# Performance work log

Hardware: AMD Instinct MI355X
Metric: run time of the kernel (lower is better)

The kernel has to match this reference:

```python
import jax, jax.numpy as jnp
import numpy as np

EMB_DIM = 1024
HEAD_DIM = 64
NUM_HEADS = EMB_DIM // HEAD_DIM  # 16
BATCH = 2
SEQ = 2048


def setup_inputs() -> dict:
    key = jax.random.key(0)
    ks = jax.random.split(key, 8)
    s = 0.02
    return {
        "q": jax.random.normal(ks[0], (BATCH, SEQ, EMB_DIM), dtype=jnp.float32),
        "k": jax.random.normal(ks[1], (BATCH, SEQ, EMB_DIM), dtype=jnp.float32),
        "v": jax.random.normal(ks[2], (BATCH, SEQ, EMB_DIM), dtype=jnp.float32),
        "W_q": jax.random.normal(ks[3], (HEAD_DIM, HEAD_DIM), dtype=jnp.float32) * s,
        "W_k": jax.random.normal(ks[4], (HEAD_DIM, HEAD_DIM), dtype=jnp.float32) * s,
        "W_v": jax.random.normal(ks[5], (HEAD_DIM, HEAD_DIM), dtype=jnp.float32) * s,
        "W_fc": jax.random.normal(ks[6], (EMB_DIM, EMB_DIM), dtype=jnp.float32) * s,
        "b_fc": jax.random.normal(ks[7], (EMB_DIM,), dtype=jnp.float32) * s,
    }


def reference(q, k, v, W_q, W_k, W_v, W_fc, b_fc):
    b = v.shape[0]
    # split into heads: [B, S, H, D]
    qh = q.reshape(b, -1, NUM_HEADS, HEAD_DIM)
    kh = k.reshape(b, -1, NUM_HEADS, HEAD_DIM)
    vh = v.reshape(b, -1, NUM_HEADS, HEAD_DIM)
    # per-head shared projections (nn.Linear: x @ W.T, no bias)
    qh = jnp.einsum('bshd,ed->bshe', qh, W_q)
    kh = jnp.einsum('bshd,ed->bshe', kh, W_k)
    vh = jnp.einsum('bshd,ed->bshe', vh, W_v)
    # scores: [B, Q, K, H]
    attn = jnp.einsum('nqhd,nkhd->nqkh', qh, kh)
    # NOTE (faithful to source): softmax over the HEADS axis (dim=3),
    # and scale by sqrt(emb_dim), not sqrt(head_dim).
    attn = jax.nn.softmax(attn / jnp.sqrt(jnp.float32(EMB_DIM)), axis=3)
    # weighted values: [B, Q, H, D] -> [B, Q, EMB]
    out = jnp.einsum('nqkh,nkhd->nqhd', attn, vh).reshape(b, -1, EMB_DIM)
    return out @ W_fc.T + b_fc
```

## Files before the change

### kernel.cpp

```cpp
#include <hip/hip_runtime.h>
#include <hip/hip_bf16.h>

#define S_LEN 2048
#define NHEAD 16
#define HDIM 64
#define EMB 1024

typedef short v8s __attribute__((ext_vector_type(8)));
typedef float v4f __attribute__((ext_vector_type(4)));

__device__ __forceinline__ float bflo(unsigned u) {
    union { unsigned u; float f; } v; v.u = u << 16; return v.f;
}
__device__ __forceinline__ float bfhi(unsigned u) {
    union { unsigned u; float f; } v; v.u = u & 0xFFFF0000u; return v.f;
}
__device__ __forceinline__ unsigned cvtpk(float lo, float hi) {
    union { __hip_bfloat162 h2; unsigned u; } v;
    float2 f; f.x = lo; f.y = hi;
    v.h2 = __float22bfloat162_rn(f);
    return v.u;
}
__device__ __forceinline__ unsigned short f2bf(float f) {
    return (unsigned short)cvtpk(f, f);
}
__device__ __forceinline__ v8s cvt8(float4 a, float4 b) {
    v8s r;
    ((unsigned*)&r)[0] = cvtpk(a.x, a.y);
    ((unsigned*)&r)[1] = cvtpk(a.z, a.w);
    ((unsigned*)&r)[2] = cvtpk(b.x, b.y);
    ((unsigned*)&r)[3] = cvtpk(b.z, b.w);
    return r;
}

__global__ __launch_bounds__(128) void k_proj2(
    const float* __restrict__ q, const float* __restrict__ k, const float* __restrict__ v,
    const float* __restrict__ Wq, const float* __restrict__ Wk, const float* __restrict__ Wv,
    unsigned short* __restrict__ Qp, unsigned short* __restrict__ Kp, unsigned short* __restrict__ Vt)
{
    __shared__ unsigned short Tq[2][16][72];
    const int t = threadIdx.x, wave = t >> 6, lane = t & 63;
    const int l15 = lane & 15, l4 = lane >> 4;
    const int mtx = blockIdx.y;
    const int hq = blockIdx.z;
    const int row0 = blockIdx.x * 32 + wave * 16;
    const int b = row0 >> 11, s0 = row0 & 2047;
    const float* X = (mtx == 0) ? q : (mtx == 1) ? k : v;
    const float* W = (mtx == 0) ? Wq : (mtx == 1) ? Wk : Wv;

    v8s wf[4][2];
    #pragma unroll
    for (int tile = 0; tile < 4; ++tile)
        #pragma unroll
        for (int c2 = 0; c2 < 2; ++c2) {
            const float* wp = W + (tile * 16 + l15) * 64 + c2 * 32 + l4 * 8;
            wf[tile][c2] = cvt8(*(const float4*)wp, *(const float4*)(wp + 4));
        }

    #pragma unroll
    for (int hi = 0; hi < 4; ++hi) {
        const int h = hq * 4 + hi;
        v8s xf[2];
        #pragma unroll
        for (int c2 = 0; c2 < 2; ++c2) {
            const float* xp = X + (size_t)(row0 + l15) * EMB + h * 64 + c2 * 32 + l4 * 8;
            xf[c2] = cvt8(*(const float4*)xp, *(const float4*)(xp + 4));
        }
        v4f acc[4];
        #pragma unroll
        for (int i = 0; i < 4; ++i) acc[i] = (v4f){0.f, 0.f, 0.f, 0.f};
        if (mtx < 2) {
            #pragma unroll
            for (int ns = 0; ns < 4; ++ns)
                #pragma unroll
                for (int c2 = 0; c2 < 2; ++c2)
                    acc[ns] = __builtin_amdgcn_mfma_f32_16x16x32_bf16(xf[c2], wf[ns][c2], acc[ns], 0, 0, 0);
            #pragma unroll
            for (int ns = 0; ns < 4; ++ns)
                #pragma unroll
                for (int r = 0; r < 4; ++r)
                    Tq[wave][l4 * 4 + r][ns * 16 + l15] = f2bf(acc[ns][r]);
            const int row = lane >> 2, c8 = (lane & 3) * 16;
            uint4 d0 = *(const uint4*)&Tq[wave][row][c8];
            uint4 d1 = *(const uint4*)&Tq[wave][row][c8 + 8];
            unsigned short* dst = ((mtx == 0) ? Qp : Kp)
                + (size_t)(b * NHEAD + h) * S_LEN * HDIM + (size_t)(s0 + row) * HDIM + c8;
            *(uint4*)dst = d0;
            *(uint4*)(dst + 8) = d1;
        } else {
            #pragma unroll
            for (int ms = 0; ms < 4; ++ms)
                #pragma unroll
                for (int c2 = 0; c2 < 2; ++c2)
                    acc[ms] = __builtin_amdgcn_mfma_f32_16x16x32_bf16(wf[ms][c2], xf[c2], acc[ms], 0, 0, 0);
            unsigned short* dst = Vt + (size_t)(b * NHEAD + h) * HDIM * S_LEN;
            #pragma unroll
            for (int ms = 0; ms < 4; ++ms)
                #pragma unroll
                for (int r = 0; r < 4; ++r)
                    dst[(size_t)(ms * 16 + l4 * 4 + r) * S_LEN + s0 + l15] = f2bf(acc[ms][r]);
        }
    }
}

__global__ __launch_bounds__(256) void k_cvtw(
    const float* __restrict__ W, unsigned short* __restrict__ Wb)
{
    const int i = (blockIdx.x * 256 + threadIdx.x) * 4;
    float4 wv = *(const float4*)(W + i);
    uint2 pk;
    pk.x = cvtpk(wv.x, wv.y);
    pk.y = cvtpk(wv.z, wv.w);
    *(uint2*)(Wb + i) = pk;
}

__global__ __launch_bounds__(1024, 4) void k_fattn(
    const unsigned short* __restrict__ Qp, const unsigned short* __restrict__ Kp,
    const unsigned short* __restrict__ Vt, unsigned short* __restrict__ Op)
{
    __shared__ unsigned short Pex[16][64][40];
    __shared__ unsigned ZrsU[64][20];
    const int t = threadIdx.x, wave = t >> 6, lane = t & 63;
    const int l15 = lane & 15, l4 = lane >> 4;
    const int h = wave;
    const int id = blockIdx.x;
    const int slot = id & 7;
    const int kqb = slot & 3;
    const int bsel = slot >> 2;
    const int qt = bsel * 32 + (id >> 3);
    const int b = qt >> 5;
    const int q0 = (qt & 31) * 64;
    const unsigned short* qh = Qp + (size_t)(b * NHEAD + h) * S_LEN * HDIM;
    const unsigned short* kh = Kp + (size_t)(b * NHEAD + h) * S_LEN * HDIM;
    const unsigned short* vh = Vt + (size_t)(b * NHEAD + h) * HDIM * S_LEN;

    v8s aq[4][2];
    #pragma unroll
    for (int qs = 0; qs < 4; ++qs)
        #pragma unroll
        for (int c2 = 0; c2 < 2; ++c2)
            aq[qs][c2] = *(const v8s*)(qh + (size_t)(q0 + qs * 16 + l15) * HDIM + c2 * 32 + l4 * 8);

    v4f o[4][4];
    #pragma unroll
    for (int qs = 0; qs < 4; ++qs)
        #pragma unroll
        for (int ds = 0; ds < 4; ++ds)
            o[qs][ds] = (v4f){0.f, 0.f, 0.f, 0.f};

    const int zq = t >> 4;
    const int zc = t & 15;

    for (int c = 0; c < 16; ++c) {
        const int kk0 = kqb * 512 + c * 32;
        #pragma unroll
        for (int ks = 0; ks < 2; ++ks) {
            const unsigned short* kb = kh + (size_t)(kk0 + ks * 16 + l15) * HDIM + l4 * 8;
            v8s b0 = *(const v8s*)kb;
            v8s b1 = *(const v8s*)(kb + 32);
            #pragma unroll
            for (int qs = 0; qs < 4; ++qs) {
                v4f sf = (v4f){0.f, 0.f, 0.f, 0.f};
                sf = __builtin_amdgcn_mfma_f32_16x16x32_bf16(aq[qs][0], b0, sf, 0, 0, 0);
                sf = __builtin_amdgcn_mfma_f32_16x16x32_bf16(aq[qs][1], b1, sf, 0, 0, 0);
                const int rb = qs * 16 + l4 * 4;
                unsigned p01 = cvtpk(__expf(sf[0] * 0.03125f), __expf(sf[1] * 0.03125f));
                unsigned p23 = cvtpk(__expf(sf[2] * 0.03125f), __expf(sf[3] * 0.03125f));
                Pex[h][rb + 0][ks * 16 + l15] = (unsigned short)p01;
                Pex[h][rb + 1][ks * 16 + l15] = (unsigned short)(p01 >> 16);
                Pex[h][rb + 2][ks * 16 + l15] = (unsigned short)p23;
                Pex[h][rb + 3][ks * 16 + l15] = (unsigned short)(p23 >> 16);
            }
        }
        __syncthreads();
        {
            float z0 = 0.f, z1 = 0.f;
            #pragma unroll
            for (int hh = 0; hh < 16; ++hh) {
                unsigned u = *(const unsigned*)&Pex[hh][zq][zc * 2];
                z0 += bflo(u); z1 += bfhi(u);
            }
            ZrsU[zq][zc] = cvtpk(__builtin_amdgcn_rcpf(z0), __builtin_amdgcn_rcpf(z1));
        }
        __syncthreads();
        {
            v8s bv[4];
            #pragma unroll
            for (int ds = 0; ds < 4; ++ds)
                bv[ds] = *(const v8s*)(vh + (size_t)(ds * 16 + l15) * S_LEN + kk0 + l4 * 8);
            #pragma unroll
            for (int qs = 0; qs < 4; ++qs) {
                uint4 pu = *(const uint4*)&Pex[h][qs * 16 + l15][l4 * 8];
                uint4 zv = *(const uint4*)&ZrsU[qs * 16 + l15][l4 * 4];
                v8s pn;
                ((unsigned*)&pn)[0] = cvtpk(bflo(pu.x) * bflo(zv.x), bfhi(pu.x) * bfhi(zv.x));
                ((unsigned*)&pn)[1] = cvtpk(bflo(pu.y) * bflo(zv.y), bfhi(pu.y) * bfhi(zv.y));
                ((unsigned*)&pn)[2] = cvtpk(bflo(pu.z) * bflo(zv.z), bfhi(pu.z) * bfhi(zv.z));
                ((unsigned*)&pn)[3] = cvtpk(bflo(pu.w) * bflo(zv.w), bfhi(pu.w) * bfhi(zv.w));
                #pragma unroll
                for (int ds = 0; ds < 4; ++ds)
                    o[qs][ds] = __builtin_amdgcn_mfma_f32_16x16x32_bf16(pn, bv[ds], o[qs][ds], 0, 0, 0);
            }
        }
    }

    unsigned short* op = Op + (size_t)(kqb * 2 + b) * S_LEN * EMB;
    #pragma unroll
    for (int qs = 0; qs < 4; ++qs)
        #pragma unroll
        for (int ds = 0; ds < 4; ++ds)
            #pragma unroll
            for (int r = 0; r < 4; ++r)
                op[(size_t)(q0 + qs * 16 + l4 * 4 + r) * EMB + h * 64 + ds * 16 + l15] =
                    f2bf(o[qs][ds][r]);
}

__global__ __launch_bounds__(256) void k_merge4(
    const unsigned short* __restrict__ Op, unsigned short* __restrict__ AO)
{
    const size_t i = ((size_t)blockIdx.x * 256 + threadIdx.x) * 8;
    const size_t row = i >> 10;
    const int b = (int)(row >> 11);
    const size_t off = (row & 2047) * EMB + (i & 1023);
    float a0 = 0, a1 = 0, a2 = 0, a3 = 0, a4 = 0, a5 = 0, a6 = 0, a7 = 0;
    #pragma unroll
    for (int kq = 0; kq < 4; ++kq) {
        uint4 u = *(const uint4*)(Op + (size_t)(kq * 2 + b) * S_LEN * EMB + off);
        a0 += bflo(u.x); a1 += bfhi(u.x);
        a2 += bflo(u.y); a3 += bfhi(u.y);
        a4 += bflo(u.z); a5 += bfhi(u.z);
        a6 += bflo(u.w); a7 += bfhi(u.w);
    }
    uint4 r;
    r.x = cvtpk(a0, a1); r.y = cvtpk(a2, a3);
    r.z = cvtpk(a4, a5); r.w = cvtpk(a6, a7);
    *(uint4*)(AO + i) = r;
}

__global__ __launch_bounds__(256) void k_fc(
    const unsigned short* __restrict__ AO, const unsigned short* __restrict__ Wb,
    const float* __restrict__ bias, float* __restrict__ out)
{
    const int t = threadIdx.x, wave = t >> 6, lane = t & 63;
    const int l15 = lane & 15, l4 = lane >> 4;
    const int m0 = blockIdx.x * 128 + wave * 32;
    const int n0 = blockIdx.y * 64;
    v4f c[2][4];
    #pragma unroll
    for (int i = 0; i < 2; ++i)
        #pragma unroll
        for (int j = 0; j < 4; ++j) c[i][j] = (v4f){0.f, 0.f, 0.f, 0.f};
    for (int k = 0; k < EMB; k += 32) {
        v8s a0 = *(const v8s*)(AO + (size_t)(m0 + l15) * EMB + k + l4 * 8);
        v8s a1 = *(const v8s*)(AO + (size_t)(m0 + 16 + l15) * EMB + k + l4 * 8);
        #pragma unroll
        for (int ns = 0; ns < 4; ++ns) {
            v8s bw = *(const v8s*)(Wb + (size_t)(n0 + ns * 16 + l15) * EMB + k + l4 * 8);
            c[0][ns] = __builtin_amdgcn_mfma_f32_16x16x32_bf16(a0, bw, c[0][ns], 0, 0, 0);
            c[1][ns] = __builtin_amdgcn_mfma_f32_16x16x32_bf16(a1, bw, c[1][ns], 0, 0, 0);
        }
    }
    #pragma unroll
    for (int ms = 0; ms < 2; ++ms)
        #pragma unroll
        for (int ns = 0; ns < 4; ++ns) {
            const float bv = bias[n0 + ns * 16 + l15];
            #pragma unroll
            for (int r = 0; r < 4; ++r)
                out[(size_t)(m0 + ms * 16 + l4 * 4 + r) * EMB + n0 + ns * 16 + l15] = c[ms][ns][r] + bv;
        }
}

extern "C" void kernel_launch(void* const* d_in, const int* in_sizes, int n_in,
                              void* d_out, int out_size, void* d_ws, size_t ws_size,
                              hipStream_t stream)
{
    (void)in_sizes; (void)n_in; (void)out_size; (void)ws_size;
    const float* q   = (const float*)d_in[0];
    const float* k   = (const float*)d_in[1];
    const float* v   = (const float*)d_in[2];
    const float* Wq  = (const float*)d_in[3];
    const float* Wk  = (const float*)d_in[4];
    const float* Wv  = (const float*)d_in[5];
    const float* Wfc = (const float*)d_in[6];
    const float* bfc = (const float*)d_in[7];

    char* w = (char*)d_ws;
    unsigned short* Qp = (unsigned short*)(w);
    unsigned short* Kp = (unsigned short*)(w + (8u  << 20));
    unsigned short* Vt = (unsigned short*)(w + (16u << 20));
    unsigned short* Wb = (unsigned short*)(w + (24u << 20));
    unsigned short* Op = (unsigned short*)(w + (26u << 20));
    unsigned short* AO = Qp;

    k_proj2 <<<dim3(128, 3, 4), dim3(128),  0, stream>>>(q, k, v, Wq, Wk, Wv, Qp, Kp, Vt);
    k_cvtw  <<<dim3(1024),      dim3(256),  0, stream>>>(Wfc, Wb);
    k_fattn <<<dim3(256),       dim3(1024), 0, stream>>>(Qp, Kp, Vt, Op);
    k_merge4<<<dim3(2048),      dim3(256),  0, stream>>>(Op, AO);
    k_fc    <<<dim3(32, 16),    dim3(256),  0, stream>>>(AO, Wb, bfc, (float*)d_out);
}
```

Baseline: 278.2 us.

## Software-pipeline attention across double-buffered query halves to overlap cross-head softmax

Each 32-key chunk is split into two 32-row query halves, each with its own LDS buffer for the exponentials and the head-sum reciprocals. The schedule becomes a software pipeline: the P·V MFMAs for one half, the cross-head normalisation for the other half and the QK exponentials for the next half run between single barriers. This removes the separate barrier that used to isolate the reduction step and lets MFMA work overlap with LDS reduction. In exchange, V tiles are now loaded from global memory once per half, so twice per chunk, and only 512 threads do the reduction.

After: 347.5 us. 24.9% more time.

```diff
diff --git a/kernel.cpp b/kernel.cpp
--- a/kernel.cpp
+++ b/kernel.cpp
@@ -118,8 +118,8 @@
     const unsigned short* __restrict__ Qp, const unsigned short* __restrict__ Kp,
     const unsigned short* __restrict__ Vt, unsigned short* __restrict__ Op)
 {
-    __shared__ unsigned short Pex[16][64][40];
-    __shared__ unsigned ZrsU[64][20];
+    __shared__ unsigned short Pex[2][16][32][40];
+    __shared__ unsigned ZrsU[2][32][20];
     const int t = threadIdx.x, wave = t >> 6, lane = t & 63;
     const int l15 = lane & 15, l4 = lane >> 4;
     const int h = wave;
@@ -148,10 +148,7 @@
         for (int ds = 0; ds < 4; ++ds)
             o[qs][ds] = (v4f){0.f, 0.f, 0.f, 0.f};
 
-    const int zq = t >> 4;
-    const int zc = t & 15;
-
-    for (int c = 0; c < 16; ++c) {
+    auto PH1 = [&](int qa, int c) {
         const int kk0 = kqb * 512 + c * 32;
         #pragma unroll
         for (int ks = 0; ks < 2; ++ks) {
@@ -159,50 +156,72 @@
             v8s b0 = *(const v8s*)kb;
             v8s b1 = *(const v8s*)(kb + 32);
             #pragma unroll
-            for (int qs = 0; qs < 4; ++qs) {
+            for (int qh2 = 0; qh2 < 2; ++qh2) {
                 v4f sf = (v4f){0.f, 0.f, 0.f, 0.f};
-                sf = __builtin_amdgcn_mfma_f32_16x16x32_bf16(aq[qs][0], b0, sf, 0, 0, 0);
-                sf = __builtin_amdgcn_mfma_f32_16x16x32_bf16(aq[qs][1], b1, sf, 0, 0, 0);
-                const int rb = qs * 16 + l4 * 4;
+                sf = __builtin_amdgcn_mfma_f32_16x16x32_bf16(aq[qa * 2 + qh2][0], b0, sf, 0, 0, 0);
+                sf = __builtin_amdgcn_mfma_f32_16x16x32_bf16(aq[qa * 2 + qh2][1], b1, sf, 0, 0, 0);
+                const int rb = qh2 * 16 + l4 * 4;
                 unsigned p01 = cvtpk(__expf(sf[0] * 0.03125f), __expf(sf[1] * 0.03125f));
                 unsigned p23 = cvtpk(__expf(sf[2] * 0.03125f), __expf(sf[3] * 0.03125f));
-                Pex[h][rb + 0][ks * 16 + l15] = (unsigned short)p01;
-                Pex[h][rb + 1][ks * 16 + l15] = (unsigned short)(p01 >> 16);
-                Pex[h][rb + 2][ks * 16 + l15] = (unsigned short)p23;
-                Pex[h][rb + 3][ks * 16 + l15] = (unsigned short)(p23 >> 16);
+                Pex[qa][h][rb + 0][ks * 16 + l15] = (unsigned short)p01;
+                Pex[qa][h][rb + 1][ks * 16 + l15] = (unsigned short)(p01 >> 16);
+                Pex[qa][h][rb + 2][ks * 16 + l15] = (unsigned short)p23;
+                Pex[qa][h][rb + 3][ks * 16 + l15] = (unsigned short)(p23 >> 16);
             }
         }
+    };
+    auto PH2 = [&](int ba) {
+        if (t < 512) {
+            const int zq = t >> 4, zc = t & 15;
+            float z0a = 0.f, z0b = 0.f, z1a = 0.f, z1b = 0.f;
+            #pragma unroll
+            for (int hh = 0; hh < 16; hh += 2) {
+                unsigned ua = *(const unsigned*)&Pex[ba][hh][zq][zc * 2];
+                unsigned ub = *(const unsigned*)&Pex[ba][hh + 1][zq][zc * 2];
+                z0a += bflo(ua); z1a += bfhi(ua);
+                z0b += bflo(ub); z1b += bfhi(ub);
+            }
+            ZrsU[ba][zq][zc] = cvtpk(__builtin_amdgcn_rcpf(z0a + z0b),
+                                     __builtin_amdgcn_rcpf(z1a + z1b));
+        }
+    };
+    auto PH3 = [&](int qa, int c) {
+        const int kk0 = kqb * 512 + c * 32;
+        v8s pn[2];
+        #pragma unroll
+        for (int qh2 = 0; qh2 < 2; ++qh2) {
+            uint4 pu = *(const uint4*)&Pex[qa][h][qh2 * 16 + l15][l4 * 8];
+            uint4 zv = *(const uint4*)&ZrsU[qa][qh2 * 16 + l15][l4 * 4];
+            ((unsigned*)&pn[qh2])[0] = cvtpk(bflo(pu.x) * bflo(zv.x), bfhi(pu.x) * bfhi(zv.x));
+            ((unsigned*)&pn[qh2])[1] = cvtpk(bflo(pu.y) * bflo(zv.y), bfhi(pu.y) * bfhi(zv.y));
+            ((unsigned*)&pn[qh2])[2] = cvtpk(bflo(pu.z) * bflo(zv.z), bfhi(pu.z) * bfhi(zv.z));
+            ((unsigned*)&pn[qh2])[3] = cvtpk(bflo(pu.w) * bflo(zv.w), bfhi(pu.w) * bfhi(zv.w));
+        }
+        #pragma unroll
+        for (int ds = 0; ds < 4; ++ds) {
+            v8s bv = *(const v8s*)(vh + (size_t)(ds * 16 + l15) * S_LEN + kk0 + l4 * 8);
+            o[qa * 2 + 0][ds] = __builtin_amdgcn_mfma_f32_16x16x32_bf16(pn[0], bv, o[qa * 2 + 0][ds], 0, 0, 0);
+            o[qa * 2 + 1][ds] = __builtin_amdgcn_mfma_f32_16x16x32_bf16(pn[1], bv, o[qa * 2 + 1][ds], 0, 0, 0);
+        }
+    };
+
+    PH1(0, 0);
+    __syncthreads();
+    PH2(0);
+    PH1(1, 0);
+    __syncthreads();
+    #pragma unroll 2
+    for (int s = 1; s < 31; ++s) {
+        const int ba = s & 1, qo = 1 - ba;
+        PH3(qo, (s - 1) >> 1);
+        PH2(ba);
+        PH1(qo, (s + 1) >> 1);
         __syncthreads();
-        {
-            float z0 = 0.f, z1 = 0.f;
-            #pragma unroll
-            for (int hh = 0; hh < 16; ++hh) {
-                unsigned u = *(const unsigned*)&Pex[hh][zq][zc * 2];
-                z0 += bflo(u); z1 += bfhi(u);
-            }
-            ZrsU[zq][zc] = cvtpk(__builtin_amdgcn_rcpf(z0), __builtin_amdgcn_rcpf(z1));
-        }
-        __syncthreads();
-        {
-            v8s bv[4];
-            #pragma unroll
-            for (int ds = 0; ds < 4; ++ds)
-                bv[ds] = *(const v8s*)(vh + (size_t)(ds * 16 + l15) * S_LEN + kk0 + l4 * 8);
-            #pragma unroll
-            for (int qs = 0; qs < 4; ++qs) {
-                uint4 pu = *(const uint4*)&Pex[h][qs * 16 + l15][l4 * 8];
-                uint4 zv = *(const uint4*)&ZrsU[qs * 16 + l15][l4 * 4];
-                v8s pn;
-                ((unsigned*)&pn)[0] = cvtpk(bflo(pu.x) * bflo(zv.x), bfhi(pu.x) * bfhi(zv.x));
-                ((unsigned*)&pn)[1] = cvtpk(bflo(pu.y) * bflo(zv.y), bfhi(pu.y) * bfhi(zv.y));
-                ((unsigned*)&pn)[2] = cvtpk(bflo(pu.z) * bflo(zv.z), bfhi(pu.z) * bfhi(zv.z));
-                ((unsigned*)&pn)[3] = cvtpk(bflo(pu.w) * bflo(zv.w), bfhi(pu.w) * bfhi(zv.w));
-                #pragma unroll
-                for (int ds = 0; ds < 4; ++ds)
-                    o[qs][ds] = __builtin_amdgcn_mfma_f32_16x16x32_bf16(pn, bv[ds], o[qs][ds], 0, 0, 0);
-            }
-        }
     }
+    PH3(0, 15);
+    PH2(1);
+    __syncthreads();
+    PH3(1, 15);
 
     unsigned short* op = Op + (size_t)(kqb * 2 + b) * S_LEN * EMB;
     #pragma unroll
```

## Fuse split-K merge into FC GEMM and weight conversion into projection

Applied to the files above, without the earlier changes.

The separate merge kernel that summed four partial attention outputs is removed. The FC GEMM now loads the four bf16 partials directly and sums them while building its A fragments. The FC weight conversion moves into extra blocks of the projection kernel, which drops two launches and the AO round-trip through memory. In exchange, each FC block re-reads and re-sums the partials once per N tile (16 times), so A-operand traffic and ALU work inside the GEMM go up.

After: 317.6 us. 1.14x slower.

```diff
diff --git a/kernel.cpp b/kernel.cpp
--- a/kernel.cpp
+++ b/kernel.cpp
@@ -36,12 +36,29 @@
 __global__ __launch_bounds__(128) void k_proj2(
     const float* __restrict__ q, const float* __restrict__ k, const float* __restrict__ v,
     const float* __restrict__ Wq, const float* __restrict__ Wk, const float* __restrict__ Wv,
-    unsigned short* __restrict__ Qp, unsigned short* __restrict__ Kp, unsigned short* __restrict__ Vt)
+    const float* __restrict__ Wfc,
+    unsigned short* __restrict__ Qp, unsigned short* __restrict__ Kp,
+    unsigned short* __restrict__ Vt, unsigned short* __restrict__ Wb)
 {
     __shared__ unsigned short Tq[2][16][72];
     const int t = threadIdx.x, wave = t >> 6, lane = t & 63;
+    const int mtx = blockIdx.y;
+
+    if (mtx == 3) {
+        const int bi = blockIdx.x * 4 + blockIdx.z;
+        const int i = (bi * 128 + t) * 16;
+        #pragma unroll
+        for (int j = 0; j < 16; j += 4) {
+            float4 wv = *(const float4*)(Wfc + i + j);
+            uint2 pk;
+            pk.x = cvtpk(wv.x, wv.y);
+            pk.y = cvtpk(wv.z, wv.w);
+            *(uint2*)(Wb + i + j) = pk;
+        }
+        return;
+    }
+
     const int l15 = lane & 15, l4 = lane >> 4;
-    const int mtx = blockIdx.y;
     const int hq = blockIdx.z;
     const int row0 = blockIdx.x * 32 + wave * 16;
     const int b = row0 >> 11, s0 = row0 & 2047;
@@ -101,17 +118,6 @@
                     dst[(size_t)(ms * 16 + l4 * 4 + r) * S_LEN + s0 + l15] = f2bf(acc[ms][r]);
         }
     }
-}
-
-__global__ __launch_bounds__(256) void k_cvtw(
-    const float* __restrict__ W, unsigned short* __restrict__ Wb)
-{
-    const int i = (blockIdx.x * 256 + threadIdx.x) * 4;
-    float4 wv = *(const float4*)(W + i);
-    uint2 pk;
-    pk.x = cvtpk(wv.x, wv.y);
-    pk.y = cvtpk(wv.z, wv.w);
-    *(uint2*)(Wb + i) = pk;
 }
 
 __global__ __launch_bounds__(1024, 4) void k_fattn(
@@ -215,44 +221,43 @@
                     f2bf(o[qs][ds][r]);
 }
 
-__global__ __launch_bounds__(256) void k_merge4(
-    const unsigned short* __restrict__ Op, unsigned short* __restrict__ AO)
-{
-    const size_t i = ((size_t)blockIdx.x * 256 + threadIdx.x) * 8;
-    const size_t row = i >> 10;
-    const int b = (int)(row >> 11);
-    const size_t off = (row & 2047) * EMB + (i & 1023);
-    float a0 = 0, a1 = 0, a2 = 0, a3 = 0, a4 = 0, a5 = 0, a6 = 0, a7 = 0;
-    #pragma unroll
-    for (int kq = 0; kq < 4; ++kq) {
-        uint4 u = *(const uint4*)(Op + (size_t)(kq * 2 + b) * S_LEN * EMB + off);
-        a0 += bflo(u.x); a1 += bfhi(u.x);
-        a2 += bflo(u.y); a3 += bfhi(u.y);
-        a4 += bflo(u.z); a5 += bfhi(u.z);
-        a6 += bflo(u.w); a7 += bfhi(u.w);
-    }
-    uint4 r;
-    r.x = cvtpk(a0, a1); r.y = cvtpk(a2, a3);
-    r.z = cvtpk(a4, a5); r.w = cvtpk(a6, a7);
-    *(uint4*)(AO + i) = r;
+__device__ __forceinline__ v8s ld_sum4(const unsigned short* __restrict__ p) {
+    const size_t po = (size_t)2 * S_LEN * EMB;
+    uint4 u0 = *(const uint4*)(p);
+    uint4 u1 = *(const uint4*)(p + po);
+    uint4 u2 = *(const uint4*)(p + 2 * po);
+    uint4 u3 = *(const uint4*)(p + 3 * po);
+    v8s r;
+    ((unsigned*)&r)[0] = cvtpk(bflo(u0.x) + bflo(u1.x) + bflo(u2.x) + bflo(u3.x),
+                               bfhi(u0.x) + bfhi(u1.x) + bfhi(u2.x) + bfhi(u3.x));
+    ((unsigned*)&r)[1] = cvtpk(bflo(u0.y) + bflo(u1.y) + bflo(u2.y) + bflo(u3.y),
+                               bfhi(u0.y) + bfhi(u1.y) + bfhi(u2.y) + bfhi(u3.y));
+    ((unsigned*)&r)[2] = cvtpk(bflo(u0.z) + bflo(u1.z) + bflo(u2.z) + bflo(u3.z),
+                               bfhi(u0.z) + bfhi(u1.z) + bfhi(u2.z) + bfhi(u3.z));
+    ((unsigned*)&r)[3] = cvtpk(bflo(u0.w) + bflo(u1.w) + bflo(u2.w) + bflo(u3.w),
+                               bfhi(u0.w) + bfhi(u1.w) + bfhi(u2.w) + bfhi(u3.w));
+    return r;
 }
 
 __global__ __launch_bounds__(256) void k_fc(
-    const unsigned short* __restrict__ AO, const unsigned short* __restrict__ Wb,
+    const unsigned short* __restrict__ Op, const unsigned short* __restrict__ Wb,
     const float* __restrict__ bias, float* __restrict__ out)
 {
     const int t = threadIdx.x, wave = t >> 6, lane = t & 63;
     const int l15 = lane & 15, l4 = lane >> 4;
     const int m0 = blockIdx.x * 128 + wave * 32;
     const int n0 = blockIdx.y * 64;
+    const int b = m0 >> 11;
+    const int s0 = m0 & 2047;
+    const unsigned short* pa = Op + (size_t)b * S_LEN * EMB;
     v4f c[2][4];
     #pragma unroll
     for (int i = 0; i < 2; ++i)
         #pragma unroll
         for (int j = 0; j < 4; ++j) c[i][j] = (v4f){0.f, 0.f, 0.f, 0.f};
     for (int k = 0; k < EMB; k += 32) {
-        v8s a0 = *(const v8s*)(AO + (size_t)(m0 + l15) * EMB + k + l4 * 8);
-        v8s a1 = *(const v8s*)(AO + (size_t)(m0 + 16 + l15) * EMB + k + l4 * 8);
+        v8s a0 = ld_sum4(pa + (size_t)(s0 + l15) * EMB + k + l4 * 8);
+        v8s a1 = ld_sum4(pa + (size_t)(s0 + 16 + l15) * EMB + k + l4 * 8);
         #pragma unroll
         for (int ns = 0; ns < 4; ++ns) {
             v8s bw = *(const v8s*)(Wb + (size_t)(n0 + ns * 16 + l15) * EMB + k + l4 * 8);
@@ -291,11 +296,8 @@
     unsigned short* Vt = (unsigned short*)(w + (16u << 20));
     unsigned short* Wb = (unsigned short*)(w + (24u << 20));
     unsigned short* Op = (unsigned short*)(w + (26u << 20));
-    unsigned short* AO = Qp;
-
-    k_proj2 <<<dim3(128, 3, 4), dim3(128),  0, stream>>>(q, k, v, Wq, Wk, Wv, Qp, Kp, Vt);
-    k_cvtw  <<<dim3(1024),      dim3(256),  0, stream>>>(Wfc, Wb);
+
+    k_proj2 <<<dim3(128, 4, 4), dim3(128),  0, stream>>>(q, k, v, Wq, Wk, Wv, Wfc, Qp, Kp, Vt, Wb);
     k_fattn <<<dim3(256),       dim3(1024), 0, stream>>>(Qp, Kp, Vt, Op);
-    k_merge4<<<dim3(2048),      dim3(256),  0, stream>>>(Op, AO);
-    k_fc    <<<dim3(32, 16),    dim3(256),  0, stream>>>(AO, Wb, bfc, (float*)d_out);
-}
+    k_fc    <<<dim3(32, 16),    dim3(256),  0, stream>>>(Op, Wb, bfc, (float*)d_out);
+}
```

## Fold FC weight conversion into projection kernel and shrink FC tiles

Applied to the files above, without the earlier changes.

Removes the separate weight-cast kernel launch by giving the projection kernel an extra grid slice (mtx==3) that converts W_fc to bf16. Each of the 512 extra blocks converts 2048 elements, which covers the full 1024x1024 matrix. The shared staging buffer is given a per-head slot so the four head iterations no longer reuse the same LDS region. The FC GEMM tile is halved to 16 rows per wave, doubling the grid to raise occupancy and parallelism, at the cost of reloading the weight tile in twice as many blocks.

New measurement: 304.0 us. 9.3% more time.

```diff
diff --git a/kernel.cpp b/kernel.cpp
--- a/kernel.cpp
+++ b/kernel.cpp
@@ -36,12 +36,29 @@
 __global__ __launch_bounds__(128) void k_proj2(
     const float* __restrict__ q, const float* __restrict__ k, const float* __restrict__ v,
     const float* __restrict__ Wq, const float* __restrict__ Wk, const float* __restrict__ Wv,
-    unsigned short* __restrict__ Qp, unsigned short* __restrict__ Kp, unsigned short* __restrict__ Vt)
-{
-    __shared__ unsigned short Tq[2][16][72];
+    const float* __restrict__ Wfc,
+    unsigned short* __restrict__ Qp, unsigned short* __restrict__ Kp,
+    unsigned short* __restrict__ Vt, unsigned short* __restrict__ Wb)
+{
+    __shared__ unsigned short Tq[2][4][16][72];
     const int t = threadIdx.x, wave = t >> 6, lane = t & 63;
+    const int mtx = blockIdx.y;
+
+    if (mtx == 3) {
+        const int bi = blockIdx.x * 4 + blockIdx.z;
+        const int i = (bi * 128 + t) * 16;
+        #pragma unroll
+        for (int j = 0; j < 16; j += 4) {
+            float4 wv = *(const float4*)(Wfc + i + j);
+            uint2 pk;
+            pk.x = cvtpk(wv.x, wv.y);
+            pk.y = cvtpk(wv.z, wv.w);
+            *(uint2*)(Wb + i + j) = pk;
+        }
+        return;
+    }
+
     const int l15 = lane & 15, l4 = lane >> 4;
-    const int mtx = blockIdx.y;
     const int hq = blockIdx.z;
     const int row0 = blockIdx.x * 32 + wave * 16;
     const int b = row0 >> 11, s0 = row0 & 2047;
@@ -79,10 +96,10 @@
             for (int ns = 0; ns < 4; ++ns)
                 #pragma unroll
                 for (int r = 0; r < 4; ++r)
-                    Tq[wave][l4 * 4 + r][ns * 16 + l15] = f2bf(acc[ns][r]);
+                    Tq[wave][hi][l4 * 4 + r][ns * 16 + l15] = f2bf(acc[ns][r]);
             const int row = lane >> 2, c8 = (lane & 3) * 16;
-            uint4 d0 = *(const uint4*)&Tq[wave][row][c8];
-            uint4 d1 = *(const uint4*)&Tq[wave][row][c8 + 8];
+            uint4 d0 = *(const uint4*)&Tq[wave][hi][row][c8];
+            uint4 d1 = *(const uint4*)&Tq[wave][hi][row][c8 + 8];
             unsigned short* dst = ((mtx == 0) ? Qp : Kp)
                 + (size_t)(b * NHEAD + h) * S_LEN * HDIM + (size_t)(s0 + row) * HDIM + c8;
             *(uint4*)dst = d0;
@@ -101,17 +118,6 @@
                     dst[(size_t)(ms * 16 + l4 * 4 + r) * S_LEN + s0 + l15] = f2bf(acc[ms][r]);
         }
     }
-}
-
-__global__ __launch_bounds__(256) void k_cvtw(
-    const float* __restrict__ W, unsigned short* __restrict__ Wb)
-{
-    const int i = (blockIdx.x * 256 + threadIdx.x) * 4;
-    float4 wv = *(const float4*)(W + i);
-    uint2 pk;
-    pk.x = cvtpk(wv.x, wv.y);
-    pk.y = cvtpk(wv.z, wv.w);
-    *(uint2*)(Wb + i) = pk;
 }
 
 __global__ __launch_bounds__(1024, 4) void k_fattn(
@@ -243,32 +249,27 @@
 {
     const int t = threadIdx.x, wave = t >> 6, lane = t & 63;
     const int l15 = lane & 15, l4 = lane >> 4;
-    const int m0 = blockIdx.x * 128 + wave * 32;
+    const int m0 = blockIdx.x * 64 + wave * 16;
     const int n0 = blockIdx.y * 64;
-    v4f c[2][4];
-    #pragma unroll
-    for (int i = 0; i < 2; ++i)
-        #pragma unroll
-        for (int j = 0; j < 4; ++j) c[i][j] = (v4f){0.f, 0.f, 0.f, 0.f};
+    v4f c[4];
+    #pragma unroll
+    for (int j = 0; j < 4; ++j) c[j] = (v4f){0.f, 0.f, 0.f, 0.f};
+    #pragma unroll 2
     for (int k = 0; k < EMB; k += 32) {
         v8s a0 = *(const v8s*)(AO + (size_t)(m0 + l15) * EMB + k + l4 * 8);
-        v8s a1 = *(const v8s*)(AO + (size_t)(m0 + 16 + l15) * EMB + k + l4 * 8);
         #pragma unroll
         for (int ns = 0; ns < 4; ++ns) {
             v8s bw = *(const v8s*)(Wb + (size_t)(n0 + ns * 16 + l15) * EMB + k + l4 * 8);
-            c[0][ns] = __builtin_amdgcn_mfma_f32_16x16x32_bf16(a0, bw, c[0][ns], 0, 0, 0);
-            c[1][ns] = __builtin_amdgcn_mfma_f32_16x16x32_bf16(a1, bw, c[1][ns], 0, 0, 0);
-        }
-    }
-    #pragma unroll
-    for (int ms = 0; ms < 2; ++ms)
-        #pragma unroll
-        for (int ns = 0; ns < 4; ++ns) {
-            const float bv = bias[n0 + ns * 16 + l15];
-            #pragma unroll
-            for (int r = 0; r < 4; ++r)
-                out[(size_t)(m0 + ms * 16 + l4 * 4 + r) * EMB + n0 + ns * 16 + l15] = c[ms][ns][r] + bv;
-        }
+            c[ns] = __builtin_amdgcn_mfma_f32_16x16x32_bf16(a0, bw, c[ns], 0, 0, 0);
+        }
+    }
+    #pragma unroll
+    for (int ns = 0; ns < 4; ++ns) {
+        const float bv = bias[n0 + ns * 16 + l15];
+        #pragma unroll
+        for (int r = 0; r < 4; ++r)
+            out[(size_t)(m0 + l4 * 4 + r) * EMB + n0 + ns * 16 + l15] = c[ns][r] + bv;
+    }
 }
 
 extern "C" void kernel_launch(void* const* d_in, const int* in_sizes, int n_in,
@@ -293,9 +294,8 @@
     unsigned short* Op = (unsigned short*)(w + (26u << 20));
     unsigned short* AO = Qp;
 
-    k_proj2 <<<dim3(128, 3, 4), dim3(128),  0, stream>>>(q, k, v, Wq, Wk, Wv, Qp, Kp, Vt);
-    k_cvtw  <<<dim3(1024),      dim3(256),  0, stream>>>(Wfc, Wb);
+    k_proj2 <<<dim3(128, 4, 4), dim3(128),  0, stream>>>(q, k, v, Wq, Wk, Wv, Wfc, Qp, Kp, Vt, Wb);
     k_fattn <<<dim3(256),       dim3(1024), 0, stream>>>(Qp, Kp, Vt, Op);
     k_merge4<<<dim3(2048),      dim3(256),  0, stream>>>(Op, AO);
-    k_fc    <<<dim3(32, 16),    dim3(256),  0, stream>>>(AO, Wb, bfc, (float*)d_out);
-}
+    k_fc    <<<dim3(64, 16),    dim3(256),  0, stream>>>(AO, Wb, bfc, (float*)d_out);
+}
```
